# Kernel optimization log

Measured on AMD Instinct MI355X. Metric: run time of the kernel, lower is better.

Reference implementation:

```python
import jax, jax.numpy as jnp
import numpy as np

N_NODES = 100000

def gcn_conv(x, W, b, src, dst, n_nodes):
    # PyG GCNConv: out = D^{-1/2} (A + I) D^{-1/2} (x W) + b, deg includes self-loop
    h = x @ W  # [N, H]
    ones = jnp.ones(src.shape[0], dtype=x.dtype)
    deg = jax.ops.segment_sum(ones, dst, num_segments=n_nodes) + 1.0  # +1 self-loop
    dinv = jax.lax.rsqrt(deg)  # deg >= 1, no zeros
    norm = dinv[src] * dinv[dst]  # [E]
    msg = h[src] * norm[:, None]  # [E, H] gather + scale
    agg = jax.ops.segment_sum(msg, dst, num_segments=n_nodes)  # scatter-add
    self_contrib = h * (dinv * dinv)[:, None]  # self-loop term norm = dinv_i^2
    return agg + self_contrib + b


def setup_inputs() -> dict:
    key = jax.random.key(0)
    ks = jax.random.split(key, 6)
    F_IN, H, E = 128, 128, 1600000
    x = jax.random.normal(ks[0], (N_NODES, F_IN), dtype=jnp.float32)
    edge_index = jax.random.randint(ks[1], (2, E), 0, N_NODES, dtype=jnp.int32)
    s = 1.0 / np.sqrt(F_IN)
    W1 = jax.random.normal(ks[2], (F_IN, H), dtype=jnp.float32) * s
    b1 = jnp.zeros((H,), dtype=jnp.float32)
    W2 = jax.random.normal(ks[3], (H, H), dtype=jnp.float32) * (1.0 / np.sqrt(H))
    b2 = jnp.zeros((H,), dtype=jnp.float32)
    Wlin = jax.random.normal(ks[4], (H, 1), dtype=jnp.float32) * (1.0 / np.sqrt(H))
    blin = jnp.zeros((1,), dtype=jnp.float32)
    return {"x": x, "edge_index": edge_index, "W1": W1, "b1": b1,
            "W2": W2, "b2": b2, "Wlin": Wlin, "blin": blin}


def reference(x, edge_index, W1, b1, W2, b2, Wlin, blin):
    src, dst = edge_index[0], edge_index[1]
    h = gcn_conv(x, W1, b1, src, dst, N_NODES)
    h = jax.nn.relu(h)
    h = gcn_conv(h, W2, b2, src, dst, N_NODES)
    h = jax.nn.relu(h)
    out = h @ Wlin + blin  # [N, 1]
    return out.squeeze(-1)  # [N]
```

## Files before the change

kernel.cpp:

```cpp
#include <hip/hip_runtime.h>
#include <hip/hip_fp16.h>

#define NFEAT 128

typedef _Float16 v8hf __attribute__((ext_vector_type(8)));
typedef float v4f __attribute__((ext_vector_type(4)));

__global__ void k_deg_rank_w(const int* __restrict__ dst, int* __restrict__ deg,
                             int* __restrict__ rank, int E, int N,
                             const float* __restrict__ W1, const float* __restrict__ W2,
                             _Float16* __restrict__ Wt1, _Float16* __restrict__ Wt2) {
  int e = blockIdx.x * blockDim.x + threadIdx.x;
  if (e < E) rank[e] = atomicAdd(&deg[dst[e]], 1);
  else if (e < E + N) rank[e] = atomicAdd(&deg[e - E], 1);
  else if (e < E + N + 32768) {
    int idx = e - E - N;
    const float* W = (idx < 16384) ? W1 : W2;
    _Float16* Wt = (idx < 16384) ? Wt1 : Wt2;
    int i = idx & 16383;
    int k = i >> 7, n = i & 127;
    Wt[n * 128 + k] = (_Float16)W[k * 128 + n];
  }
}

__global__ __launch_bounds__(1024) void k_scan_blocks(const int* __restrict__ deg,
    int* __restrict__ base, int* __restrict__ partials, int n) {
  __shared__ int buf[1024];
  int tid = threadIdx.x;
  int i = blockIdx.x * 1024 + tid;
  int v = (i < n) ? deg[i] : 0;
  buf[tid] = v;
  __syncthreads();
  #pragma unroll
  for (int off = 1; off < 1024; off <<= 1) {
    int t = (tid >= off) ? buf[tid - off] : 0;
    __syncthreads();
    buf[tid] += t;
    __syncthreads();
  }
  if (i <= n) base[i] = buf[tid] - v;
  if (tid == 1023) partials[blockIdx.x] = buf[tid];
}

__global__ void k_scan_partials(int* __restrict__ partials, int nb) {
  __shared__ int buf[128];
  int tid = threadIdx.x;
  int v = (tid < nb) ? partials[tid] : 0;
  buf[tid] = v;
  __syncthreads();
  #pragma unroll
  for (int off = 1; off < 128; off <<= 1) {
    int t = (tid >= off) ? buf[tid - off] : 0;
    __syncthreads();
    buf[tid] += t;
    __syncthreads();
  }
  if (tid < nb) partials[tid] = buf[tid] - v;
}

__global__ void k_finalize_base(int* __restrict__ base, const int* __restrict__ partials,
    const int* __restrict__ deg, float* __restrict__ dinv, int n) {
  int i = blockIdx.x * blockDim.x + threadIdx.x;
  if (i <= n) {
    base[i] += partials[i >> 10];
    if (i < n) dinv[i] = rsqrtf((float)deg[i]);
  }
}

__global__ void k_scatter(const int* __restrict__ src, const int* __restrict__ dst,
    const int* __restrict__ rank, const int* __restrict__ base,
    int* __restrict__ ssrc, int E, int N) {
  int e = blockIdx.x * blockDim.x + threadIdx.x;
  if (e < E) ssrc[base[dst[e]] + rank[e]] = src[e];
  else if (e < E + N) { int n = e - E; ssrc[base[n] + rank[e]] = n; }
}

template <typename AT>
__global__ __launch_bounds__(256) void k_gemm_mfma(
    const AT* __restrict__ A, const _Float16* __restrict__ Wt,
    const float* __restrict__ dinv, _Float16* __restrict__ g16, int N) {
  __shared__ _Float16 As[64][136];
  __shared__ _Float16 Ws[128][136];
  const int tid = threadIdx.x;
  const int row0 = blockIdx.x * 64;

  if (blockIdx.x == 0 && tid < 16) {
    v8hf z;
    #pragma unroll
    for (int j = 0; j < 8; j++) z[j] = (_Float16)0.f;
    *(v8hf*)(g16 + (size_t)N * NFEAT + tid * 8) = z;
  }

  if constexpr (sizeof(AT) == 4) {
    #pragma unroll
    for (int i = 0; i < 8; i++) {
      int idx = tid + i * 256;
      int row = idx >> 5;
      int c4 = idx & 31;
      int gr = row0 + row; gr = (gr < N) ? gr : (N - 1);
      float4 v = *(const float4*)((const float*)A + (size_t)gr * NFEAT + c4 * 4);
      _Float16* p = &As[row][c4 * 4];
      p[0] = (_Float16)v.x; p[1] = (_Float16)v.y;
      p[2] = (_Float16)v.z; p[3] = (_Float16)v.w;
    }
  } else {
    #pragma unroll
    for (int i = 0; i < 4; i++) {
      int idx = tid + i * 256;
      int row = idx >> 4;
      int c8 = idx & 15;
      int gr = row0 + row; gr = (gr < N) ? gr : (N - 1);
      *(uint4*)&As[row][c8 * 8] =
          *(const uint4*)((const _Float16*)A + (size_t)gr * NFEAT + c8 * 8);
    }
  }
  #pragma unroll
  for (int i = 0; i < 8; i++) {
    int idx = tid + i * 256;
    int row = idx >> 4;
    int c8 = idx & 15;
    *(uint4*)&Ws[row][c8 * 8] = *(const uint4*)(Wt + (size_t)row * 128 + c8 * 8);
  }
  __syncthreads();

  const int wv = tid >> 6;
  const int lane = tid & 63;
  const int m = lane & 15;
  const int q = lane >> 4;

  v4f acc[8] = {};
  const _Float16* arow = &As[wv * 16 + m][0];
  #pragma unroll
  for (int kt = 0; kt < 4; kt++) {
    v8hf af = *(const v8hf*)(arow + kt * 32 + q * 8);
    #pragma unroll
    for (int ct = 0; ct < 8; ct++) {
      v8hf bf = *(const v8hf*)(&Ws[ct * 16 + m][kt * 32 + q * 8]);
      acc[ct] = __builtin_amdgcn_mfma_f32_16x16x32_f16(af, bf, acc[ct], 0, 0, 0);
    }
  }

  int nd[4]; float dv[4];
  #pragma unroll
  for (int r = 0; r < 4; r++) {
    nd[r] = row0 + wv * 16 + q * 4 + r;
    int c = (nd[r] < N) ? nd[r] : (N - 1);
    dv[r] = dinv[c];
  }
  #pragma unroll
  for (int ct = 0; ct < 8; ct++)
    #pragma unroll
    for (int r = 0; r < 4; r++)
      if (nd[r] < N)
        g16[(size_t)nd[r] * NFEAT + ct * 16 + m] = (_Float16)(acc[ct][r] * dv[r]);
}

__global__ __launch_bounds__(256) void k_agg(
    const _Float16* __restrict__ g, const float* __restrict__ dinv,
    const int* __restrict__ base, const int* __restrict__ ssrc,
    const float* __restrict__ bias, _Float16* __restrict__ hB, int N) {
  const int lane = threadIdx.x & 63;
  const int n = blockIdx.x * 4 + (threadIdx.x >> 6);
  if (n >= N) return;
  const int gq = lane >> 4;
  const int l = lane & 15;
  const int b0 = base[n], b1 = base[n + 1];

  int e = b0;
  int p0 = e + gq, p1 = e + 4 + gq;
  int i0 = ssrc[p0], i1 = ssrc[p1];
  i0 = (p0 < b1) ? i0 : N;
  i1 = (p1 < b1) ? i1 : N;
  v8hf r0 = *(const v8hf*)(g + (size_t)i0 * NFEAT + l * 8);
  v8hf r1 = *(const v8hf*)(g + (size_t)i1 * NFEAT + l * 8);
  int e2 = e + 8;
  int j0 = N, j1 = N;
  if (e2 < b1) {
    int q0 = e2 + gq, q1 = e2 + 4 + gq;
    j0 = ssrc[q0]; j1 = ssrc[q1];
    j0 = (q0 < b1) ? j0 : N;
    j1 = (q1 < b1) ? j1 : N;
  }

  float acc[8] = {};
  while (true) {
    bool more = (e2 < b1);
    v8hf s0, s1;
    if (more) {
      s0 = *(const v8hf*)(g + (size_t)j0 * NFEAT + l * 8);
      s1 = *(const v8hf*)(g + (size_t)j1 * NFEAT + l * 8);
    }
    int e3 = e2 + 8;
    int c0 = N, c1 = N;
    if (e3 < b1) {
      int q0 = e3 + gq, q1 = e3 + 4 + gq;
      c0 = ssrc[q0]; c1 = ssrc[q1];
      c0 = (q0 < b1) ? c0 : N;
      c1 = (q1 < b1) ? c1 : N;
    }
    #pragma unroll
    for (int j = 0; j < 8; j++) acc[j] += (float)r0[j] + (float)r1[j];
    if (!more) break;
    r0 = s0; r1 = s1;
    j0 = c0; j1 = c1;
    e2 = e3;
  }

  #pragma unroll
  for (int j = 0; j < 8; j++) {
    acc[j] += __shfl_xor(acc[j], 16, 64);
    acc[j] += __shfl_xor(acc[j], 32, 64);
  }
  if (gq == 0) {
    float dvn = dinv[n];
    const float* bp = bias + l * 8;
    float4 bb0 = *(const float4*)(bp);
    float4 bb1 = *(const float4*)(bp + 4);
    float bv[8] = {bb0.x, bb0.y, bb0.z, bb0.w, bb1.x, bb1.y, bb1.z, bb1.w};
    v8hf o;
    #pragma unroll
    for (int j = 0; j < 8; j++)
      o[j] = (_Float16)fmaxf(acc[j] * dvn + bv[j], 0.f);
    *(v8hf*)(hB + (size_t)n * NFEAT + l * 8) = o;
  }
}

__global__ __launch_bounds__(256) void k_agg_final(
    const _Float16* __restrict__ g, const float* __restrict__ dinv,
    const int* __restrict__ base, const int* __restrict__ ssrc,
    const float* __restrict__ bias, const float* __restrict__ wlin,
    const float* __restrict__ blin, float* __restrict__ out, int N) {
  const int lane = threadIdx.x & 63;
  const int n = blockIdx.x * 4 + (threadIdx.x >> 6);
  if (n >= N) return;
  const int gq = lane >> 4;
  const int l = lane & 15;
  const int b0 = base[n], b1 = base[n + 1];

  int e = b0;
  int p0 = e + gq, p1 = e + 4 + gq;
  int i0 = ssrc[p0], i1 = ssrc[p1];
  i0 = (p0 < b1) ? i0 : N;
  i1 = (p1 < b1) ? i1 : N;
  v8hf r0 = *(const v8hf*)(g + (size_t)i0 * NFEAT + l * 8);
  v8hf r1 = *(const v8hf*)(g + (size_t)i1 * NFEAT + l * 8);
  int e2 = e + 8;
  int j0 = N, j1 = N;
  if (e2 < b1) {
    int q0 = e2 + gq, q1 = e2 + 4 + gq;
    j0 = ssrc[q0]; j1 = ssrc[q1];
    j0 = (q0 < b1) ? j0 : N;
    j1 = (q1 < b1) ? j1 : N;
  }

  float acc[8] = {};
  while (true) {
    bool more = (e2 < b1);
    v8hf s0, s1;
    if (more) {
      s0 = *(const v8hf*)(g + (size_t)j0 * NFEAT + l * 8);
      s1 = *(const v8hf*)(g + (size_t)j1 * NFEAT + l * 8);
    }
    int e3 = e2 + 8;
    int c0 = N, c1 = N;
    if (e3 < b1) {
      int q0 = e3 + gq, q1 = e3 + 4 + gq;
      c0 = ssrc[q0]; c1 = ssrc[q1];
      c0 = (q0 < b1) ? c0 : N;
      c1 = (q1 < b1) ? c1 : N;
    }
    #pragma unroll
    for (int j = 0; j < 8; j++) acc[j] += (float)r0[j] + (float)r1[j];
    if (!more) break;
    r0 = s0; r1 = s1;
    j0 = c0; j1 = c1;
    e2 = e3;
  }

  #pragma unroll
  for (int j = 0; j < 8; j++) {
    acc[j] += __shfl_xor(acc[j], 16, 64);
    acc[j] += __shfl_xor(acc[j], 32, 64);
  }
  float dvn = dinv[n];
  const float* bp = bias + l * 8;
  const float* wp = wlin + l * 8;
  float4 bb0 = *(const float4*)(bp);
  float4 bb1 = *(const float4*)(bp + 4);
  float4 wl0 = *(const float4*)(wp);
  float4 wl1 = *(const float4*)(wp + 4);
  float bv[8] = {bb0.x, bb0.y, bb0.z, bb0.w, bb1.x, bb1.y, bb1.z, bb1.w};
  float wv[8] = {wl0.x, wl0.y, wl0.z, wl0.w, wl1.x, wl1.y, wl1.z, wl1.w};
  float pv = 0.f;
  #pragma unroll
  for (int j = 0; j < 8; j++)
    pv += fmaxf(acc[j] * dvn + bv[j], 0.f) * wv[j];
  pv += __shfl_xor(pv, 1, 64);
  pv += __shfl_xor(pv, 2, 64);
  pv += __shfl_xor(pv, 4, 64);
  pv += __shfl_xor(pv, 8, 64);
  if (lane == 0) out[n] = pv + blin[0];
}

extern "C" void kernel_launch(void* const* d_in, const int* in_sizes, int n_in,
                              void* d_out, int out_size, void* d_ws, size_t ws_size,
                              hipStream_t stream) {
  const float* x    = (const float*)d_in[0];
  const int*   ei   = (const int*)d_in[1];
  const float* W1   = (const float*)d_in[2];
  const float* b1   = (const float*)d_in[3];
  const float* W2   = (const float*)d_in[4];
  const float* b2   = (const float*)d_in[5];
  const float* Wlin = (const float*)d_in[6];
  const float* blin = (const float*)d_in[7];
  const int N = in_sizes[0] / NFEAT;
  const int E = in_sizes[1] / 2;
  const int* src = ei;
  const int* dst = ei + E;
  const int Etot = E + N;

  int* ws_i = (int*)d_ws;
  size_t off = 0;
  int* deg      = ws_i + off; off += N;
  int* base     = ws_i + off; off += (size_t)N + 1;
  off = (off + 3) & ~(size_t)3;
  int* partials = ws_i + off; off += 128;
  int* ssrc     = ws_i + off; off += Etot + 8;
  float* dinv   = (float*)(ws_i + off); off += N;
  off = (off + 3) & ~(size_t)3;
  _Float16* Wt1 = (_Float16*)(ws_i + off); off += 8192;
  _Float16* Wt2 = (_Float16*)(ws_i + off); off += 8192;
  _Float16* g16 = (_Float16*)(ws_i + off); off += (size_t)(N + 1) * 64;
  _Float16* hB  = (_Float16*)(ws_i + off); off += (size_t)N * 64;
  int* rank     = (int*)g16;

  hipMemsetAsync(deg, 0, (size_t)N * sizeof(int), stream);

  const int tpbE = 256;
  const int gE = (Etot + 32768 + tpbE - 1) / tpbE;
  k_deg_rank_w<<<gE, tpbE, 0, stream>>>(dst, deg, rank, E, N, W1, W2, Wt1, Wt2);

  const int nb = (N + 1 + 1023) / 1024;
  k_scan_blocks<<<nb, 1024, 0, stream>>>(deg, base, partials, N);
  k_scan_partials<<<1, 128, 0, stream>>>(partials, nb);
  k_finalize_base<<<((N + 1) + 255) / 256, 256, 0, stream>>>(base, partials, deg, dinv, N);
  k_scatter<<<(Etot + tpbE - 1) / tpbE, tpbE, 0, stream>>>(src, dst, rank, base, ssrc, E, N);

  const int gg = (N + 63) / 64;
  const int ga = (N + 3) / 4;
  k_gemm_mfma<float><<<gg, 256, 0, stream>>>(x, Wt1, dinv, g16, N);
  k_agg<<<ga, 256, 0, stream>>>(g16, dinv, base, ssrc, b1, hB, N);
  k_gemm_mfma<_Float16><<<gg, 256, 0, stream>>>(hB, Wt2, dinv, g16, N);
  k_agg_final<<<ga, 256, 0, stream>>>(g16, dinv, base, ssrc, b2,
                                      Wlin, blin, (float*)d_out, N);
}
```

Measured before the change: 383.3 us.

## Split gathered features into 16-wide column chunks for cache-local aggregation

The GEMM output is stored as eight column-chunk planes of 16 features each, and the aggregation kernels run one block per chunk, covering 16 nodes, so every gather touches a 32-byte row segment within a smaller per-chunk working set. The aim is better L2 hit rates on the random neighbor gathers, since each chunk plane is an eighth of the full feature matrix. In exchange, the index array is re-read once per chunk, the final layer needs an output memset plus atomic adds across chunks, and the per-wave loop runs to the maximum degree among the four nodes it handles.

```diff
diff --git a/kernel.cpp b/kernel.cpp
--- a/kernel.cpp
+++ b/kernel.cpp
@@ -2,6 +2,8 @@
 #include <hip/hip_fp16.h>
 
 #define NFEAT 128
+#define NCHUNK 8
+#define CFEAT 16
 
 typedef _Float16 v8hf __attribute__((ext_vector_type(8)));
 typedef float v4f __attribute__((ext_vector_type(4)));
@@ -88,7 +90,8 @@
     v8hf z;
     #pragma unroll
     for (int j = 0; j < 8; j++) z[j] = (_Float16)0.f;
-    *(v8hf*)(g16 + (size_t)N * NFEAT + tid * 8) = z;
+    int c = tid >> 1, h = tid & 1;
+    *(v8hf*)(g16 + ((size_t)c * (N + 1) + N) * CFEAT + h * 8) = z;
   }
 
   if constexpr (sizeof(AT) == 4) {
@@ -148,80 +151,79 @@
     dv[r] = dinv[c];
   }
   #pragma unroll
-  for (int ct = 0; ct < 8; ct++)
+  for (int ct = 0; ct < 8; ct++) {
+    _Float16* gout = g16 + (size_t)ct * (N + 1) * CFEAT;
     #pragma unroll
     for (int r = 0; r < 4; r++)
       if (nd[r] < N)
-        g16[(size_t)nd[r] * NFEAT + ct * 16 + m] = (_Float16)(acc[ct][r] * dv[r]);
+        gout[(size_t)nd[r] * CFEAT + m] = (_Float16)(acc[ct][r] * dv[r]);
+  }
 }
 
 __global__ __launch_bounds__(256) void k_agg(
     const _Float16* __restrict__ g, const float* __restrict__ dinv,
     const int* __restrict__ base, const int* __restrict__ ssrc,
     const float* __restrict__ bias, _Float16* __restrict__ hB, int N) {
+  const int chunk = blockIdx.x & 7;
+  const int nblk = blockIdx.x >> 3;
   const int lane = threadIdx.x & 63;
-  const int n = blockIdx.x * 4 + (threadIdx.x >> 6);
-  if (n >= N) return;
-  const int gq = lane >> 4;
-  const int l = lane & 15;
-  const int b0 = base[n], b1 = base[n + 1];
-
-  int e = b0;
-  int p0 = e + gq, p1 = e + 4 + gq;
-  int i0 = ssrc[p0], i1 = ssrc[p1];
-  i0 = (p0 < b1) ? i0 : N;
-  i1 = (p1 < b1) ? i1 : N;
-  v8hf r0 = *(const v8hf*)(g + (size_t)i0 * NFEAT + l * 8);
-  v8hf r1 = *(const v8hf*)(g + (size_t)i1 * NFEAT + l * 8);
-  int e2 = e + 8;
-  int j0 = N, j1 = N;
-  if (e2 < b1) {
-    int q0 = e2 + gq, q1 = e2 + 4 + gq;
-    j0 = ssrc[q0]; j1 = ssrc[q1];
-    j0 = (q0 < b1) ? j0 : N;
-    j1 = (q1 < b1) ? j1 : N;
-  }
+  const int wave = threadIdx.x >> 6;
+  const int half = lane & 1;
+  const int slot = (lane >> 1) & 7;
+  const int n = nblk * 16 + wave * 4 + (lane >> 4);
+
+  const _Float16* gc = g + (size_t)chunk * (N + 1) * CFEAT;
+
+  int b0 = 0, b1 = 0;
+  if (n < N) { b0 = base[n]; b1 = base[n + 1]; }
+  int nit = (b1 - b0 + 7) >> 3;
+  { int t = __shfl_xor(nit, 16, 64); nit = (t > nit) ? t : nit; }
+  { int t = __shfl_xor(nit, 32, 64); nit = (t > nit) ? t : nit; }
 
   float acc[8] = {};
-  while (true) {
-    bool more = (e2 < b1);
-    v8hf s0, s1;
-    if (more) {
-      s0 = *(const v8hf*)(g + (size_t)j0 * NFEAT + l * 8);
-      s1 = *(const v8hf*)(g + (size_t)j1 * NFEAT + l * 8);
-    }
-    int e3 = e2 + 8;
-    int c0 = N, c1 = N;
-    if (e3 < b1) {
-      int q0 = e3 + gq, q1 = e3 + 4 + gq;
-      c0 = ssrc[q0]; c1 = ssrc[q1];
-      c0 = (q0 < b1) ? c0 : N;
-      c1 = (q1 < b1) ? c1 : N;
-    }
-    #pragma unroll
-    for (int j = 0; j < 8; j++) acc[j] += (float)r0[j] + (float)r1[j];
-    if (!more) break;
-    r0 = s0; r1 = s1;
-    j0 = c0; j1 = c1;
-    e2 = e3;
-  }
-
-  #pragma unroll
-  for (int j = 0; j < 8; j++) {
-    acc[j] += __shfl_xor(acc[j], 16, 64);
-    acc[j] += __shfl_xor(acc[j], 32, 64);
-  }
-  if (gq == 0) {
+  if (nit > 0) {
+    int p = b0 + slot;
+    int i = ssrc[p];
+    i = (p < b1) ? i : N;
+    v8hf r = *(const v8hf*)(gc + (size_t)i * CFEAT + half * 8);
+    int j = N;
+    if (nit > 1) {
+      int pn = b0 + 8 + slot;
+      j = ssrc[pn];
+      j = (pn < b1) ? j : N;
+    }
+    for (int it = 1; ; ++it) {
+      bool more = (it < nit);
+      v8hf rn; int jn = N;
+      if (more) {
+        rn = *(const v8hf*)(gc + (size_t)j * CFEAT + half * 8);
+        if (it + 1 < nit) {
+          int pn = b0 + (it + 1) * 8 + slot;
+          jn = ssrc[pn];
+          jn = (pn < b1) ? jn : N;
+        }
+      }
+      #pragma unroll
+      for (int jj = 0; jj < 8; jj++) acc[jj] += (float)r[jj];
+      if (!more) break;
+      r = rn; j = jn;
+    }
+  }
+
+  #pragma unroll
+  for (int jj = 0; jj < 8; jj++) {
+    acc[jj] += __shfl_xor(acc[jj], 2, 64);
+    acc[jj] += __shfl_xor(acc[jj], 4, 64);
+    acc[jj] += __shfl_xor(acc[jj], 8, 64);
+  }
+  if (n < N && (lane & 14) == 0) {
     float dvn = dinv[n];
-    const float* bp = bias + l * 8;
-    float4 bb0 = *(const float4*)(bp);
-    float4 bb1 = *(const float4*)(bp + 4);
-    float bv[8] = {bb0.x, bb0.y, bb0.z, bb0.w, bb1.x, bb1.y, bb1.z, bb1.w};
+    const float* bp = bias + chunk * CFEAT + half * 8;
     v8hf o;
     #pragma unroll
-    for (int j = 0; j < 8; j++)
-      o[j] = (_Float16)fmaxf(acc[j] * dvn + bv[j], 0.f);
-    *(v8hf*)(hB + (size_t)n * NFEAT + l * 8) = o;
+    for (int jj = 0; jj < 8; jj++)
+      o[jj] = (_Float16)fmaxf(acc[jj] * dvn + bp[jj], 0.f);
+    *(v8hf*)(hB + (size_t)n * NFEAT + chunk * CFEAT + half * 8) = o;
   }
 }
 
@@ -230,76 +232,72 @@
     const int* __restrict__ base, const int* __restrict__ ssrc,
     const float* __restrict__ bias, const float* __restrict__ wlin,
     const float* __restrict__ blin, float* __restrict__ out, int N) {
+  const int chunk = blockIdx.x & 7;
+  const int nblk = blockIdx.x >> 3;
   const int lane = threadIdx.x & 63;
-  const int n = blockIdx.x * 4 + (threadIdx.x >> 6);
-  if (n >= N) return;
-  const int gq = lane >> 4;
-  const int l = lane & 15;
-  const int b0 = base[n], b1 = base[n + 1];
-
-  int e = b0;
-  int p0 = e + gq, p1 = e + 4 + gq;
-  int i0 = ssrc[p0], i1 = ssrc[p1];
-  i0 = (p0 < b1) ? i0 : N;
-  i1 = (p1 < b1) ? i1 : N;
-  v8hf r0 = *(const v8hf*)(g + (size_t)i0 * NFEAT + l * 8);
-  v8hf r1 = *(const v8hf*)(g + (size_t)i1 * NFEAT + l * 8);
-  int e2 = e + 8;
-  int j0 = N, j1 = N;
-  if (e2 < b1) {
-    int q0 = e2 + gq, q1 = e2 + 4 + gq;
-    j0 = ssrc[q0]; j1 = ssrc[q1];
-    j0 = (q0 < b1) ? j0 : N;
-    j1 = (q1 < b1) ? j1 : N;
-  }
+  const int wave = threadIdx.x >> 6;
+  const int half = lane & 1;
+  const int slot = (lane >> 1) & 7;
+  const int n = nblk * 16 + wave * 4 + (lane >> 4);
+
+  const _Float16* gc = g + (size_t)chunk * (N + 1) * CFEAT;
+
+  int b0 = 0, b1 = 0;
+  if (n < N) { b0 = base[n]; b1 = base[n + 1]; }
+  int nit = (b1 - b0 + 7) >> 3;
+  { int t = __shfl_xor(nit, 16, 64); nit = (t > nit) ? t : nit; }
+  { int t = __shfl_xor(nit, 32, 64); nit = (t > nit) ? t : nit; }
 
   float acc[8] = {};
-  while (true) {
-    bool more = (e2 < b1);
-    v8hf s0, s1;
-    if (more) {
-      s0 = *(const v8hf*)(g + (size_t)j0 * NFEAT + l * 8);
-      s1 = *(const v8hf*)(g + (size_t)j1 * NFEAT + l * 8);
-    }
-    int e3 = e2 + 8;
-    int c0 = N, c1 = N;
-    if (e3 < b1) {
-      int q0 = e3 + gq, q1 = e3 + 4 + gq;
-      c0 = ssrc[q0]; c1 = ssrc[q1];
-      c0 = (q0 < b1) ? c0 : N;
-      c1 = (q1 < b1) ? c1 : N;
-    }
-    #pragma unroll
-    for (int j = 0; j < 8; j++) acc[j] += (float)r0[j] + (float)r1[j];
-    if (!more) break;
-    r0 = s0; r1 = s1;
-    j0 = c0; j1 = c1;
-    e2 = e3;
-  }
-
-  #pragma unroll
-  for (int j = 0; j < 8; j++) {
-    acc[j] += __shfl_xor(acc[j], 16, 64);
-    acc[j] += __shfl_xor(acc[j], 32, 64);
-  }
-  float dvn = dinv[n];
-  const float* bp = bias + l * 8;
-  const float* wp = wlin + l * 8;
-  float4 bb0 = *(const float4*)(bp);
-  float4 bb1 = *(const float4*)(bp + 4);
-  float4 wl0 = *(const float4*)(wp);
-  float4 wl1 = *(const float4*)(wp + 4);
-  float bv[8] = {bb0.x, bb0.y, bb0.z, bb0.w, bb1.x, bb1.y, bb1.z, bb1.w};
-  float wv[8] = {wl0.x, wl0.y, wl0.z, wl0.w, wl1.x, wl1.y, wl1.z, wl1.w};
+  if (nit > 0) {
+    int p = b0 + slot;
+    int i = ssrc[p];
+    i = (p < b1) ? i : N;
+    v8hf r = *(const v8hf*)(gc + (size_t)i * CFEAT + half * 8);
+    int j = N;
+    if (nit > 1) {
+      int pn = b0 + 8 + slot;
+      j = ssrc[pn];
+      j = (pn < b1) ? j : N;
+    }
+    for (int it = 1; ; ++it) {
+      bool more = (it < nit);
+      v8hf rn; int jn = N;
+      if (more) {
+        rn = *(const v8hf*)(gc + (size_t)j * CFEAT + half * 8);
+        if (it + 1 < nit) {
+          int pn = b0 + (it + 1) * 8 + slot;
+          jn = ssrc[pn];
+          jn = (pn < b1) ? jn : N;
+        }
+      }
+      #pragma unroll
+      for (int jj = 0; jj < 8; jj++) acc[jj] += (float)r[jj];
+      if (!more) break;
+      r = rn; j = jn;
+    }
+  }
+
+  #pragma unroll
+  for (int jj = 0; jj < 8; jj++) {
+    acc[jj] += __shfl_xor(acc[jj], 2, 64);
+    acc[jj] += __shfl_xor(acc[jj], 4, 64);
+    acc[jj] += __shfl_xor(acc[jj], 8, 64);
+  }
   float pv = 0.f;
-  #pragma unroll
-  for (int j = 0; j < 8; j++)
-    pv += fmaxf(acc[j] * dvn + bv[j], 0.f) * wv[j];
+  if (n < N) {
+    float dvn = dinv[n];
+    const float* bp = bias + chunk * CFEAT + half * 8;
+    const float* wp = wlin + chunk * CFEAT + half * 8;
+    #pragma unroll
+    for (int jj = 0; jj < 8; jj++)
+      pv += fmaxf(acc[jj] * dvn + bp[jj], 0.f) * wp[jj];
+  }
   pv += __shfl_xor(pv, 1, 64);
-  pv += __shfl_xor(pv, 2, 64);
-  pv += __shfl_xor(pv, 4, 64);
-  pv += __shfl_xor(pv, 8, 64);
-  if (lane == 0) out[n] = pv + blin[0];
+  if (n < N && (lane & 15) == 0) {
+    if (chunk == 0) pv += blin[0];
+    atomicAdd(out + n, pv);
+  }
 }
 
 extern "C" void kernel_launch(void* const* d_in, const int* in_sizes, int n_in,
@@ -325,7 +323,7 @@
   int* base     = ws_i + off; off += (size_t)N + 1;
   off = (off + 3) & ~(size_t)3;
   int* partials = ws_i + off; off += 128;
-  int* ssrc     = ws_i + off; off += Etot + 8;
+  int* ssrc     = ws_i + off; off += Etot + 64;
   float* dinv   = (float*)(ws_i + off); off += N;
   off = (off + 3) & ~(size_t)3;
   _Float16* Wt1 = (_Float16*)(ws_i + off); off += 8192;
@@ -335,6 +333,7 @@
   int* rank     = (int*)g16;
 
   hipMemsetAsync(deg, 0, (size_t)N * sizeof(int), stream);
+  hipMemsetAsync(d_out, 0, (size_t)N * sizeof(float), stream);
 
   const int tpbE = 256;
   const int gE = (Etot + 32768 + tpbE - 1) / tpbE;
@@ -347,7 +346,7 @@
   k_scatter<<<(Etot + tpbE - 1) / tpbE, tpbE, 0, stream>>>(src, dst, rank, base, ssrc, E, N);
 
   const int gg = (N + 63) / 64;
-  const int ga = (N + 3) / 4;
+  const int ga = NCHUNK * ((N + 15) >> 4);
   k_gemm_mfma<float><<<gg, 256, 0, stream>>>(x, Wt1, dinv, g16, N);
   k_agg<<<ga, 256, 0, stream>>>(g16, dinv, base, ssrc, b1, hB, N);
   k_gemm_mfma<_Float16><<<gg, 256, 0, stream>>>(hB, Wt2, dinv, g16, N);
```

Result: slower. 438.7 us (+14.5%).

## Fuse all GCN stages into one cooperative persistent kernel with grid syncs

Applied to the files above, without the earlier changes.

Replaces the chain of nine kernel launches (degree/rank, three scan stages, scatter, two GEMMs, two aggregations) with a single cooperative kernel of 512 persistent blocks that loops over work and separates stages with grid.sync. The scan is redone with 512-element chunks using wave shuffles. The goal is to remove launch gaps and tail effects between the many small stages. The trade-off is a fixed grid size that limits occupancy per phase, plus grid barrier costs, and a fallback to the old launches if the cooperative launch fails.

```diff
diff --git a/kernel.cpp b/kernel.cpp
--- a/kernel.cpp
+++ b/kernel.cpp
@@ -1,10 +1,351 @@
 #include <hip/hip_runtime.h>
 #include <hip/hip_fp16.h>
+#include <hip/hip_cooperative_groups.h>
+
+namespace cg = cooperative_groups;
 
 #define NFEAT 128
+#define NBLK 512
 
 typedef _Float16 v8hf __attribute__((ext_vector_type(8)));
 typedef float v4f __attribute__((ext_vector_type(4)));
+
+__device__ __forceinline__ int wave_incl_scan(int v, int lane) {
+  #pragma unroll
+  for (int off = 1; off < 64; off <<= 1) {
+    int t = __shfl_up(v, off, 64);
+    if (lane >= off) v += t;
+  }
+  return v;
+}
+
+template <typename AT>
+__device__ __forceinline__ void gemm_tile(
+    const AT* A, const _Float16* Wt, const float* dinv,
+    _Float16* g16, int N, int tile,
+    _Float16 (*As)[136], _Float16 (*Ws)[136]) {
+  const int tid = threadIdx.x;
+  const int row0 = tile * 64;
+
+  if constexpr (sizeof(AT) == 4) {
+    #pragma unroll
+    for (int i = 0; i < 8; i++) {
+      int idx = tid + i * 256;
+      int row = idx >> 5;
+      int c4 = idx & 31;
+      int gr = row0 + row; gr = (gr < N) ? gr : (N - 1);
+      float4 v = *(const float4*)((const float*)A + (size_t)gr * NFEAT + c4 * 4);
+      _Float16* p = &As[row][c4 * 4];
+      p[0] = (_Float16)v.x; p[1] = (_Float16)v.y;
+      p[2] = (_Float16)v.z; p[3] = (_Float16)v.w;
+    }
+  } else {
+    #pragma unroll
+    for (int i = 0; i < 4; i++) {
+      int idx = tid + i * 256;
+      int row = idx >> 4;
+      int c8 = idx & 15;
+      int gr = row0 + row; gr = (gr < N) ? gr : (N - 1);
+      *(uint4*)&As[row][c8 * 8] =
+          *(const uint4*)((const _Float16*)A + (size_t)gr * NFEAT + c8 * 8);
+    }
+  }
+  #pragma unroll
+  for (int i = 0; i < 8; i++) {
+    int idx = tid + i * 256;
+    int row = idx >> 4;
+    int c8 = idx & 15;
+    *(uint4*)&Ws[row][c8 * 8] = *(const uint4*)(Wt + (size_t)row * 128 + c8 * 8);
+  }
+  __syncthreads();
+
+  const int wv = tid >> 6;
+  const int lane = tid & 63;
+  const int m = lane & 15;
+  const int q = lane >> 4;
+
+  v4f acc[8] = {};
+  const _Float16* arow = &As[wv * 16 + m][0];
+  #pragma unroll
+  for (int kt = 0; kt < 4; kt++) {
+    v8hf af = *(const v8hf*)(arow + kt * 32 + q * 8);
+    #pragma unroll
+    for (int ct = 0; ct < 8; ct++) {
+      v8hf bf = *(const v8hf*)(&Ws[ct * 16 + m][kt * 32 + q * 8]);
+      acc[ct] = __builtin_amdgcn_mfma_f32_16x16x32_f16(af, bf, acc[ct], 0, 0, 0);
+    }
+  }
+
+  int nd[4]; float dv[4];
+  #pragma unroll
+  for (int r = 0; r < 4; r++) {
+    nd[r] = row0 + wv * 16 + q * 4 + r;
+    int c = (nd[r] < N) ? nd[r] : (N - 1);
+    dv[r] = dinv[c];
+  }
+  #pragma unroll
+  for (int ct = 0; ct < 8; ct++)
+    #pragma unroll
+    for (int r = 0; r < 4; r++)
+      if (nd[r] < N)
+        g16[(size_t)nd[r] * NFEAT + ct * 16 + m] = (_Float16)(acc[ct][r] * dv[r]);
+}
+
+__device__ __forceinline__ void agg_node(
+    const _Float16* g, const float* dinv, const int* base, const int* ssrc,
+    const float* bias, _Float16* hB, int N, int n) {
+  const int lane = threadIdx.x & 63;
+  if (n >= N) return;
+  const int gq = lane >> 4;
+  const int l = lane & 15;
+  const int b0 = base[n], b1 = base[n + 1];
+
+  int e = b0;
+  int p0 = e + gq, p1 = e + 4 + gq;
+  int i0 = ssrc[p0], i1 = ssrc[p1];
+  i0 = (p0 < b1) ? i0 : N;
+  i1 = (p1 < b1) ? i1 : N;
+  v8hf r0 = *(const v8hf*)(g + (size_t)i0 * NFEAT + l * 8);
+  v8hf r1 = *(const v8hf*)(g + (size_t)i1 * NFEAT + l * 8);
+  int e2 = e + 8;
+  int j0 = N, j1 = N;
+  if (e2 < b1) {
+    int q0 = e2 + gq, q1 = e2 + 4 + gq;
+    j0 = ssrc[q0]; j1 = ssrc[q1];
+    j0 = (q0 < b1) ? j0 : N;
+    j1 = (q1 < b1) ? j1 : N;
+  }
+
+  float acc[8] = {};
+  while (true) {
+    bool more = (e2 < b1);
+    v8hf s0, s1;
+    if (more) {
+      s0 = *(const v8hf*)(g + (size_t)j0 * NFEAT + l * 8);
+      s1 = *(const v8hf*)(g + (size_t)j1 * NFEAT + l * 8);
+    }
+    int e3 = e2 + 8;
+    int c0 = N, c1 = N;
+    if (e3 < b1) {
+      int q0 = e3 + gq, q1 = e3 + 4 + gq;
+      c0 = ssrc[q0]; c1 = ssrc[q1];
+      c0 = (q0 < b1) ? c0 : N;
+      c1 = (q1 < b1) ? c1 : N;
+    }
+    #pragma unroll
+    for (int j = 0; j < 8; j++) acc[j] += (float)r0[j] + (float)r1[j];
+    if (!more) break;
+    r0 = s0; r1 = s1;
+    j0 = c0; j1 = c1;
+    e2 = e3;
+  }
+
+  #pragma unroll
+  for (int j = 0; j < 8; j++) {
+    acc[j] += __shfl_xor(acc[j], 16, 64);
+    acc[j] += __shfl_xor(acc[j], 32, 64);
+  }
+  if (gq == 0) {
+    float dvn = dinv[n];
+    const float* bp = bias + l * 8;
+    float4 bb0 = *(const float4*)(bp);
+    float4 bb1 = *(const float4*)(bp + 4);
+    float bv[8] = {bb0.x, bb0.y, bb0.z, bb0.w, bb1.x, bb1.y, bb1.z, bb1.w};
+    v8hf o;
+    #pragma unroll
+    for (int j = 0; j < 8; j++)
+      o[j] = (_Float16)fmaxf(acc[j] * dvn + bv[j], 0.f);
+    *(v8hf*)(hB + (size_t)n * NFEAT + l * 8) = o;
+  }
+}
+
+__device__ __forceinline__ void agg_final_node(
+    const _Float16* g, const float* dinv, const int* base, const int* ssrc,
+    const float* bias, const float* wlin, const float* blin,
+    float* out, int N, int n) {
+  const int lane = threadIdx.x & 63;
+  if (n >= N) return;
+  const int gq = lane >> 4;
+  const int l = lane & 15;
+  const int b0 = base[n], b1 = base[n + 1];
+
+  int e = b0;
+  int p0 = e + gq, p1 = e + 4 + gq;
+  int i0 = ssrc[p0], i1 = ssrc[p1];
+  i0 = (p0 < b1) ? i0 : N;
+  i1 = (p1 < b1) ? i1 : N;
+  v8hf r0 = *(const v8hf*)(g + (size_t)i0 * NFEAT + l * 8);
+  v8hf r1 = *(const v8hf*)(g + (size_t)i1 * NFEAT + l * 8);
+  int e2 = e + 8;
+  int j0 = N, j1 = N;
+  if (e2 < b1) {
+    int q0 = e2 + gq, q1 = e2 + 4 + gq;
+    j0 = ssrc[q0]; j1 = ssrc[q1];
+    j0 = (q0 < b1) ? j0 : N;
+    j1 = (q1 < b1) ? j1 : N;
+  }
+
+  float acc[8] = {};
+  while (true) {
+    bool more = (e2 < b1);
+    v8hf s0, s1;
+    if (more) {
+      s0 = *(const v8hf*)(g + (size_t)j0 * NFEAT + l * 8);
+      s1 = *(const v8hf*)(g + (size_t)j1 * NFEAT + l * 8);
+    }
+    int e3 = e2 + 8;
+    int c0 = N, c1 = N;
+    if (e3 < b1) {
+      int q0 = e3 + gq, q1 = e3 + 4 + gq;
+      c0 = ssrc[q0]; c1 = ssrc[q1];
+      c0 = (q0 < b1) ? c0 : N;
+      c1 = (q1 < b1) ? c1 : N;
+    }
+    #pragma unroll
+    for (int j = 0; j < 8; j++) acc[j] += (float)r0[j] + (float)r1[j];
+    if (!more) break;
+    r0 = s0; r1 = s1;
+    j0 = c0; j1 = c1;
+    e2 = e3;
+  }
+
+  #pragma unroll
+  for (int j = 0; j < 8; j++) {
+    acc[j] += __shfl_xor(acc[j], 16, 64);
+    acc[j] += __shfl_xor(acc[j], 32, 64);
+  }
+  float dvn = dinv[n];
+  const float* bp = bias + l * 8;
+  const float* wp = wlin + l * 8;
+  float4 bb0 = *(const float4*)(bp);
+  float4 bb1 = *(const float4*)(bp + 4);
+  float4 wl0 = *(const float4*)(wp);
+  float4 wl1 = *(const float4*)(wp + 4);
+  float bv[8] = {bb0.x, bb0.y, bb0.z, bb0.w, bb1.x, bb1.y, bb1.z, bb1.w};
+  float wv[8] = {wl0.x, wl0.y, wl0.z, wl0.w, wl1.x, wl1.y, wl1.z, wl1.w};
+  float pv = 0.f;
+  #pragma unroll
+  for (int j = 0; j < 8; j++)
+    pv += fmaxf(acc[j] * dvn + bv[j], 0.f) * wv[j];
+  pv += __shfl_xor(pv, 1, 64);
+  pv += __shfl_xor(pv, 2, 64);
+  pv += __shfl_xor(pv, 4, 64);
+  pv += __shfl_xor(pv, 8, 64);
+  if (lane == 0) out[n] = pv + blin[0];
+}
+
+__global__ __launch_bounds__(256, 2) void k_mega(
+    const float* __restrict__ x, const int* __restrict__ ei,
+    const float* __restrict__ W1, const float* __restrict__ b1,
+    const float* __restrict__ W2, const float* __restrict__ b2,
+    const float* __restrict__ Wlin, const float* __restrict__ blin,
+    int* deg, int* base, int* partials, int* ssrc, float* dinv,
+    _Float16* Wt1, _Float16* Wt2, _Float16* g16, _Float16* hB,
+    float* out, int E, int N) {
+  __shared__ _Float16 As[64][136];
+  __shared__ _Float16 Ws[128][136];
+  __shared__ int scan_lds[4];
+  cg::grid_group grid = cg::this_grid();
+
+  const int tid = threadIdx.x;
+  const int lane = tid & 63;
+  const int wv = tid >> 6;
+  const int gid = blockIdx.x * 256 + tid;
+  const int gstride = gridDim.x * 256;
+  const int Etot = E + N;
+  const int* src = ei;
+  const int* dst = ei + E;
+  int* rank = (int*)g16;
+
+  for (int e = gid; e < Etot + 32768; e += gstride) {
+    if (e < E) rank[e] = atomicAdd(&deg[dst[e]], 1);
+    else if (e < Etot) rank[e] = atomicAdd(&deg[e - E], 1);
+    else {
+      int idx = e - Etot;
+      const float* W = (idx < 16384) ? W1 : W2;
+      _Float16* Wt = (idx < 16384) ? Wt1 : Wt2;
+      int i = idx & 16383;
+      int k = i >> 7, nn = i & 127;
+      Wt[nn * 128 + k] = (_Float16)W[k * 128 + nn];
+    }
+  }
+  grid.sync();
+
+  const int N1 = N + 1;
+  const int nch = (N1 + 511) >> 9;
+  for (int ch = blockIdx.x; ch < nch; ch += gridDim.x) {
+    int i0 = (ch << 9) + (tid << 1);
+    int a = (i0 < N) ? deg[i0] : 0;
+    int b = (i0 + 1 < N) ? deg[i0 + 1] : 0;
+    int inc = wave_incl_scan(a + b, lane);
+    if (lane == 63) scan_lds[wv] = inc;
+    __syncthreads();
+    int woff = 0, tot = 0;
+    #pragma unroll
+    for (int w = 0; w < 4; w++) {
+      int t = scan_lds[w];
+      tot += t;
+      if (w < wv) woff += t;
+    }
+    __syncthreads();
+    int ex = woff + inc - (a + b);
+    if (i0 < N1) base[i0] = ex;
+    if (i0 + 1 < N1) base[i0 + 1] = ex + a;
+    if (tid == 0) partials[ch] = tot;
+  }
+  grid.sync();
+
+  if (blockIdx.x == 0) {
+    int v = (tid < nch) ? partials[tid] : 0;
+    int inc = wave_incl_scan(v, lane);
+    if (lane == 63) scan_lds[wv] = inc;
+    __syncthreads();
+    int woff = 0;
+    #pragma unroll
+    for (int w = 0; w < 4; w++) if (w < wv) woff += scan_lds[w];
+    if (tid < nch) partials[tid] = woff + inc - v;
+  }
+  grid.sync();
+
+  for (int i = gid; i < N1; i += gstride) {
+    base[i] += partials[i >> 9];
+    if (i < N) dinv[i] = rsqrtf((float)deg[i]);
+  }
+  if (blockIdx.x == 0 && tid < 16) {
+    v8hf z;
+    #pragma unroll
+    for (int j = 0; j < 8; j++) z[j] = (_Float16)0.f;
+    *(v8hf*)(g16 + (size_t)N * NFEAT + tid * 8) = z;
+  }
+  grid.sync();
+
+  for (int e = gid; e < Etot; e += gstride) {
+    if (e < E) ssrc[base[dst[e]] + rank[e]] = src[e];
+    else { int nn = e - E; ssrc[base[nn] + rank[e]] = nn; }
+  }
+  grid.sync();
+
+  const int ntiles = (N + 63) >> 6;
+  for (int t = blockIdx.x; t < ntiles; t += gridDim.x) {
+    __syncthreads();
+    gemm_tile<float>(x, Wt1, dinv, g16, N, t, As, Ws);
+  }
+  grid.sync();
+
+  const int ngrp = (N + 3) >> 2;
+  for (int g4 = blockIdx.x; g4 < ngrp; g4 += gridDim.x)
+    agg_node(g16, dinv, base, ssrc, b1, hB, N, g4 * 4 + wv);
+  grid.sync();
+
+  for (int t = blockIdx.x; t < ntiles; t += gridDim.x) {
+    __syncthreads();
+    gemm_tile<_Float16>(hB, Wt2, dinv, g16, N, t, As, Ws);
+  }
+  grid.sync();
+
+  for (int g4 = blockIdx.x; g4 < ngrp; g4 += gridDim.x)
+    agg_final_node(g16, dinv, base, ssrc, b2, Wlin, blin, out, N, g4 * 4 + wv);
+}
 
 __global__ void k_deg_rank_w(const int* __restrict__ dst, int* __restrict__ deg,
                              int* __restrict__ rank, int E, int N,
@@ -81,148 +422,20 @@
     const float* __restrict__ dinv, _Float16* __restrict__ g16, int N) {
   __shared__ _Float16 As[64][136];
   __shared__ _Float16 Ws[128][136];
-  const int tid = threadIdx.x;
-  const int row0 = blockIdx.x * 64;
-
-  if (blockIdx.x == 0 && tid < 16) {
+  if (blockIdx.x == 0 && threadIdx.x < 16) {
     v8hf z;
     #pragma unroll
     for (int j = 0; j < 8; j++) z[j] = (_Float16)0.f;
-    *(v8hf*)(g16 + (size_t)N * NFEAT + tid * 8) = z;
-  }
-
-  if constexpr (sizeof(AT) == 4) {
-    #pragma unroll
-    for (int i = 0; i < 8; i++) {
-      int idx = tid + i * 256;
-      int row = idx >> 5;
-      int c4 = idx & 31;
-      int gr = row0 + row; gr = (gr < N) ? gr : (N - 1);
-      float4 v = *(const float4*)((const float*)A + (size_t)gr * NFEAT + c4 * 4);
-      _Float16* p = &As[row][c4 * 4];
-      p[0] = (_Float16)v.x; p[1] = (_Float16)v.y;
-      p[2] = (_Float16)v.z; p[3] = (_Float16)v.w;
-    }
-  } else {
-    #pragma unroll
-    for (int i = 0; i < 4; i++) {
-      int idx = tid + i * 256;
-      int row = idx >> 4;
-      int c8 = idx & 15;
-      int gr = row0 + row; gr = (gr < N) ? gr : (N - 1);
-      *(uint4*)&As[row][c8 * 8] =
-          *(const uint4*)((const _Float16*)A + (size_t)gr * NFEAT + c8 * 8);
-    }
-  }
-  #pragma unroll
-  for (int i = 0; i < 8; i++) {
-    int idx = tid + i * 256;
-    int row = idx >> 4;
-    int c8 = idx & 15;
-    *(uint4*)&Ws[row][c8 * 8] = *(const uint4*)(Wt + (size_t)row * 128 + c8 * 8);
-  }
-  __syncthreads();
-
-  const int wv = tid >> 6;
-  const int lane = tid & 63;
-  const int m = lane & 15;
-  const int q = lane >> 4;
-
-  v4f acc[8] = {};
-  const _Float16* arow = &As[wv * 16 + m][0];
-  #pragma unroll
-  for (int kt = 0; kt < 4; kt++) {
-    v8hf af = *(const v8hf*)(arow + kt * 32 + q * 8);
-    #pragma unroll
-    for (int ct = 0; ct < 8; ct++) {
-      v8hf bf = *(const v8hf*)(&Ws[ct * 16 + m][kt * 32 + q * 8]);
-      acc[ct] = __builtin_amdgcn_mfma_f32_16x16x32_f16(af, bf, acc[ct], 0, 0, 0);
-    }
-  }
-
-  int nd[4]; float dv[4];
-  #pragma unroll
-  for (int r = 0; r < 4; r++) {
-    nd[r] = row0 + wv * 16 + q * 4 + r;
-    int c = (nd[r] < N) ? nd[r] : (N - 1);
-    dv[r] = dinv[c];
-  }
-  #pragma unroll
-  for (int ct = 0; ct < 8; ct++)
-    #pragma unroll
-    for (int r = 0; r < 4; r++)
-      if (nd[r] < N)
-        g16[(size_t)nd[r] * NFEAT + ct * 16 + m] = (_Float16)(acc[ct][r] * dv[r]);
+    *(v8hf*)(g16 + (size_t)N * NFEAT + threadIdx.x * 8) = z;
+  }
+  gemm_tile<AT>(A, Wt, dinv, g16, N, blockIdx.x, As, Ws);
 }
 
 __global__ __launch_bounds__(256) void k_agg(
     const _Float16* __restrict__ g, const float* __restrict__ dinv,
     const int* __restrict__ base, const int* __restrict__ ssrc,
     const float* __restrict__ bias, _Float16* __restrict__ hB, int N) {
-  const int lane = threadIdx.x & 63;
-  const int n = blockIdx.x * 4 + (threadIdx.x >> 6);
-  if (n >= N) return;
-  const int gq = lane >> 4;
-  const int l = lane & 15;
-  const int b0 = base[n], b1 = base[n + 1];
-
-  int e = b0;
-  int p0 = e + gq, p1 = e + 4 + gq;
-  int i0 = ssrc[p0], i1 = ssrc[p1];
-  i0 = (p0 < b1) ? i0 : N;
-  i1 = (p1 < b1) ? i1 : N;
-  v8hf r0 = *(const v8hf*)(g + (size_t)i0 * NFEAT + l * 8);
-  v8hf r1 = *(const v8hf*)(g + (size_t)i1 * NFEAT + l * 8);
-  int e2 = e + 8;
-  int j0 = N, j1 = N;
-  if (e2 < b1) {
-    int q0 = e2 + gq, q1 = e2 + 4 + gq;
-    j0 = ssrc[q0]; j1 = ssrc[q1];
-    j0 = (q0 < b1) ? j0 : N;
-    j1 = (q1 < b1) ? j1 : N;
-  }
-
-  float acc[8] = {};
-  while (true) {
-    bool more = (e2 < b1);
-    v8hf s0, s1;
-    if (more) {
-      s0 = *(const v8hf*)(g + (size_t)j0 * NFEAT + l * 8);
-      s1 = *(const v8hf*)(g + (size_t)j1 * NFEAT + l * 8);
-    }
-    int e3 = e2 + 8;
-    int c0 = N, c1 = N;
-    if (e3 < b1) {
-      int q0 = e3 + gq, q1 = e3 + 4 + gq;
-      c0 = ssrc[q0]; c1 = ssrc[q1];
-      c0 = (q0 < b1) ? c0 : N;
-      c1 = (q1 < b1) ? c1 : N;
-    }
-    #pragma unroll
-    for (int j = 0; j < 8; j++) acc[j] += (float)r0[j] + (float)r1[j];
-    if (!more) break;
-    r0 = s0; r1 = s1;
-    j0 = c0; j1 = c1;
-    e2 = e3;
-  }
-
-  #pragma unroll
-  for (int j = 0; j < 8; j++) {
-    acc[j] += __shfl_xor(acc[j], 16, 64);
-    acc[j] += __shfl_xor(acc[j], 32, 64);
-  }
-  if (gq == 0) {
-    float dvn = dinv[n];
-    const float* bp = bias + l * 8;
-    float4 bb0 = *(const float4*)(bp);
-    float4 bb1 = *(const float4*)(bp + 4);
-    float bv[8] = {bb0.x, bb0.y, bb0.z, bb0.w, bb1.x, bb1.y, bb1.z, bb1.w};
-    v8hf o;
-    #pragma unroll
-    for (int j = 0; j < 8; j++)
-      o[j] = (_Float16)fmaxf(acc[j] * dvn + bv[j], 0.f);
-    *(v8hf*)(hB + (size_t)n * NFEAT + l * 8) = o;
-  }
+  agg_node(g, dinv, base, ssrc, bias, hB, N, blockIdx.x * 4 + (threadIdx.x >> 6));
 }
 
 __global__ __launch_bounds__(256) void k_agg_final(
@@ -230,76 +443,8 @@
     const int* __restrict__ base, const int* __restrict__ ssrc,
     const float* __restrict__ bias, const float* __restrict__ wlin,
     const float* __restrict__ blin, float* __restrict__ out, int N) {
-  const int lane = threadIdx.x & 63;
-  const int n = blockIdx.x * 4 + (threadIdx.x >> 6);
-  if (n >= N) return;
-  const int gq = lane >> 4;
-  const int l = lane & 15;
-  const int b0 = base[n], b1 = base[n + 1];
-
-  int e = b0;
-  int p0 = e + gq, p1 = e + 4 + gq;
-  int i0 = ssrc[p0], i1 = ssrc[p1];
-  i0 = (p0 < b1) ? i0 : N;
-  i1 = (p1 < b1) ? i1 : N;
-  v8hf r0 = *(const v8hf*)(g + (size_t)i0 * NFEAT + l * 8);
-  v8hf r1 = *(const v8hf*)(g + (size_t)i1 * NFEAT + l * 8);
-  int e2 = e + 8;
-  int j0 = N, j1 = N;
-  if (e2 < b1) {
-    int q0 = e2 + gq, q1 = e2 + 4 + gq;
-    j0 = ssrc[q0]; j1 = ssrc[q1];
-    j0 = (q0 < b1) ? j0 : N;
-    j1 = (q1 < b1) ? j1 : N;
-  }
-
-  float acc[8] = {};
-  while (true) {
-    bool more = (e2 < b1);
-    v8hf s0, s1;
-    if (more) {
-      s0 = *(const v8hf*)(g + (size_t)j0 * NFEAT + l * 8);
-      s1 = *(const v8hf*)(g + (size_t)j1 * NFEAT + l * 8);
-    }
-    int e3 = e2 + 8;
-    int c0 = N, c1 = N;
-    if (e3 < b1) {
-      int q0 = e3 + gq, q1 = e3 + 4 + gq;
-      c0 = ssrc[q0]; c1 = ssrc[q1];
-      c0 = (q0 < b1) ? c0 : N;
-      c1 = (q1 < b1) ? c1 : N;
-    }
-    #pragma unroll
-    for (int j = 0; j < 8; j++) acc[j] += (float)r0[j] + (float)r1[j];
-    if (!more) break;
-    r0 = s0; r1 = s1;
-    j0 = c0; j1 = c1;
-    e2 = e3;
-  }
-
-  #pragma unroll
-  for (int j = 0; j < 8; j++) {
-    acc[j] += __shfl_xor(acc[j], 16, 64);
-    acc[j] += __shfl_xor(acc[j], 32, 64);
-  }
-  float dvn = dinv[n];
-  const float* bp = bias + l * 8;
-  const float* wp = wlin + l * 8;
-  float4 bb0 = *(const float4*)(bp);
-  float4 bb1 = *(const float4*)(bp + 4);
-  float4 wl0 = *(const float4*)(wp);
-  float4 wl1 = *(const float4*)(wp + 4);
-  float bv[8] = {bb0.x, bb0.y, bb0.z, bb0.w, bb1.x, bb1.y, bb1.z, bb1.w};
-  float wv[8] = {wl0.x, wl0.y, wl0.z, wl0.w, wl1.x, wl1.y, wl1.z, wl1.w};
-  float pv = 0.f;
-  #pragma unroll
-  for (int j = 0; j < 8; j++)
-    pv += fmaxf(acc[j] * dvn + bv[j], 0.f) * wv[j];
-  pv += __shfl_xor(pv, 1, 64);
-  pv += __shfl_xor(pv, 2, 64);
-  pv += __shfl_xor(pv, 4, 64);
-  pv += __shfl_xor(pv, 8, 64);
-  if (lane == 0) out[n] = pv + blin[0];
+  agg_final_node(g, dinv, base, ssrc, bias, wlin, blin, out, N,
+                 blockIdx.x * 4 + (threadIdx.x >> 6));
 }
 
 extern "C" void kernel_launch(void* const* d_in, const int* in_sizes, int n_in,
@@ -315,16 +460,15 @@
   const float* blin = (const float*)d_in[7];
   const int N = in_sizes[0] / NFEAT;
   const int E = in_sizes[1] / 2;
-  const int* src = ei;
-  const int* dst = ei + E;
   const int Etot = E + N;
+  float* outp = (float*)d_out;
 
   int* ws_i = (int*)d_ws;
   size_t off = 0;
   int* deg      = ws_i + off; off += N;
   int* base     = ws_i + off; off += (size_t)N + 1;
   off = (off + 3) & ~(size_t)3;
-  int* partials = ws_i + off; off += 128;
+  int* partials = ws_i + off; off += 256;
   int* ssrc     = ws_i + off; off += Etot + 8;
   float* dinv   = (float*)(ws_i + off); off += N;
   off = (off + 3) & ~(size_t)3;
@@ -336,21 +480,34 @@
 
   hipMemsetAsync(deg, 0, (size_t)N * sizeof(int), stream);
 
-  const int tpbE = 256;
-  const int gE = (Etot + 32768 + tpbE - 1) / tpbE;
-  k_deg_rank_w<<<gE, tpbE, 0, stream>>>(dst, deg, rank, E, N, W1, W2, Wt1, Wt2);
-
-  const int nb = (N + 1 + 1023) / 1024;
-  k_scan_blocks<<<nb, 1024, 0, stream>>>(deg, base, partials, N);
-  k_scan_partials<<<1, 128, 0, stream>>>(partials, nb);
-  k_finalize_base<<<((N + 1) + 255) / 256, 256, 0, stream>>>(base, partials, deg, dinv, N);
-  k_scatter<<<(Etot + tpbE - 1) / tpbE, tpbE, 0, stream>>>(src, dst, rank, base, ssrc, E, N);
-
-  const int gg = (N + 63) / 64;
-  const int ga = (N + 3) / 4;
-  k_gemm_mfma<float><<<gg, 256, 0, stream>>>(x, Wt1, dinv, g16, N);
-  k_agg<<<ga, 256, 0, stream>>>(g16, dinv, base, ssrc, b1, hB, N);
-  k_gemm_mfma<_Float16><<<gg, 256, 0, stream>>>(hB, Wt2, dinv, g16, N);
-  k_agg_final<<<ga, 256, 0, stream>>>(g16, dinv, base, ssrc, b2,
-                                      Wlin, blin, (float*)d_out, N);
-}
+  int Ea = E, Na = N;
+  void* args[] = {
+    (void*)&x, (void*)&ei, (void*)&W1, (void*)&b1, (void*)&W2, (void*)&b2,
+    (void*)&Wlin, (void*)&blin, (void*)&deg, (void*)&base, (void*)&partials,
+    (void*)&ssrc, (void*)&dinv, (void*)&Wt1, (void*)&Wt2, (void*)&g16,
+    (void*)&hB, (void*)&outp, (void*)&Ea, (void*)&Na
+  };
+  hipError_t err = hipLaunchCooperativeKernel(k_mega, dim3(NBLK), dim3(256),
+                                              args, 0, stream);
+  if (err != hipSuccess) {
+    const int* src = ei;
+    const int* dst = ei + E;
+    const int tpbE = 256;
+    const int gE = (Etot + 32768 + tpbE - 1) / tpbE;
+    k_deg_rank_w<<<gE, tpbE, 0, stream>>>(dst, deg, rank, E, N, W1, W2, Wt1, Wt2);
+
+    const int nb = (N + 1 + 1023) / 1024;
+    k_scan_blocks<<<nb, 1024, 0, stream>>>(deg, base, partials, N);
+    k_scan_partials<<<1, 128, 0, stream>>>(partials, nb);
+    k_finalize_base<<<((N + 1) + 255) / 256, 256, 0, stream>>>(base, partials, deg, dinv, N);
+    k_scatter<<<(Etot + tpbE - 1) / tpbE, tpbE, 0, stream>>>(src, dst, rank, base, ssrc, E, N);
+
+    const int gg = (N + 63) / 64;
+    const int ga = (N + 3) / 4;
+    k_gemm_mfma<float><<<gg, 256, 0, stream>>>(x, Wt1, dinv, g16, N);
+    k_agg<<<ga, 256, 0, stream>>>(g16, dinv, base, ssrc, b1, hB, N);
+    k_gemm_mfma<_Float16><<<gg, 256, 0, stream>>>(hB, Wt2, dinv, g16, N);
+    k_agg_final<<<ga, 256, 0, stream>>>(g16, dinv, base, ssrc, b2,
+                                        Wlin, blin, outp, N);
+  }
+}
```

New measurement: 964.3 us. +151.6%, slower.

## Use wave-shuffle scans and stage GEMM output through LDS for coalesced stores

Applied to the files above, without the earlier changes.

The block scan moves from an LDS Hillis-Steele loop with many barriers to 64-wide wave shuffle scans over 256-thread blocks, with each thread handling two elements. The partials scan is rewritten the same way. The GEMM epilogue now writes scaled fp16 results into shared memory and then stores 16-byte vectors per row, replacing scattered 2-byte global stores, and the fp32-to-fp16 A-tile conversion uses one vector LDS store. These changes target scan synchronisation overhead and uncoalesced GEMM writes, at the cost of two extra barriers in the GEMM.

```diff
diff --git a/kernel.cpp b/kernel.cpp
--- a/kernel.cpp
+++ b/kernel.cpp
@@ -4,6 +4,7 @@
 #define NFEAT 128
 
 typedef _Float16 v8hf __attribute__((ext_vector_type(8)));
+typedef _Float16 v4hf __attribute__((ext_vector_type(4)));
 typedef float v4f __attribute__((ext_vector_type(4)));
 
 __global__ void k_deg_rank_w(const int* __restrict__ dst, int* __restrict__ deg,
@@ -23,46 +24,62 @@
   }
 }
 
-__global__ __launch_bounds__(1024) void k_scan_blocks(const int* __restrict__ deg,
+__device__ __forceinline__ int wave_incl_scan(int v, int lane) {
+  #pragma unroll
+  for (int off = 1; off < 64; off <<= 1) {
+    int t = __shfl_up(v, off, 64);
+    if (lane >= off) v += t;
+  }
+  return v;
+}
+
+__global__ __launch_bounds__(256) void k_scan_blocks(const int* __restrict__ deg,
     int* __restrict__ base, int* __restrict__ partials, int n) {
-  __shared__ int buf[1024];
-  int tid = threadIdx.x;
-  int i = blockIdx.x * 1024 + tid;
-  int v = (i < n) ? deg[i] : 0;
-  buf[tid] = v;
-  __syncthreads();
-  #pragma unroll
-  for (int off = 1; off < 1024; off <<= 1) {
-    int t = (tid >= off) ? buf[tid - off] : 0;
-    __syncthreads();
-    buf[tid] += t;
-    __syncthreads();
-  }
-  if (i <= n) base[i] = buf[tid] - v;
-  if (tid == 1023) partials[blockIdx.x] = buf[tid];
-}
-
-__global__ void k_scan_partials(int* __restrict__ partials, int nb) {
-  __shared__ int buf[128];
-  int tid = threadIdx.x;
+  __shared__ int lds[4];
+  const int tid = threadIdx.x;
+  const int lane = tid & 63;
+  const int wv = tid >> 6;
+  int i0 = (blockIdx.x << 9) + (tid << 1);
+  int a = (i0 < n) ? deg[i0] : 0;
+  int b = (i0 + 1 < n) ? deg[i0 + 1] : 0;
+  int inc = wave_incl_scan(a + b, lane);
+  if (lane == 63) lds[wv] = inc;
+  __syncthreads();
+  int woff = 0, tot = 0;
+  #pragma unroll
+  for (int w = 0; w < 4; w++) {
+    int t = lds[w];
+    tot += t;
+    if (w < wv) woff += t;
+  }
+  int ex = woff + inc - (a + b);
+  const int N1 = n + 1;
+  if (i0 < N1) base[i0] = ex;
+  if (i0 + 1 < N1) base[i0 + 1] = ex + a;
+  if (tid == 255) partials[blockIdx.x] = tot;
+}
+
+__global__ __launch_bounds__(256) void k_scan_partials(int* __restrict__ partials,
+                                                       int nb) {
+  __shared__ int lds[4];
+  const int tid = threadIdx.x;
+  const int lane = tid & 63;
+  const int wv = tid >> 6;
   int v = (tid < nb) ? partials[tid] : 0;
-  buf[tid] = v;
-  __syncthreads();
-  #pragma unroll
-  for (int off = 1; off < 128; off <<= 1) {
-    int t = (tid >= off) ? buf[tid - off] : 0;
-    __syncthreads();
-    buf[tid] += t;
-    __syncthreads();
-  }
-  if (tid < nb) partials[tid] = buf[tid] - v;
+  int inc = wave_incl_scan(v, lane);
+  if (lane == 63) lds[wv] = inc;
+  __syncthreads();
+  int woff = 0;
+  #pragma unroll
+  for (int w = 0; w < 4; w++) if (w < wv) woff += lds[w];
+  if (tid < nb) partials[tid] = woff + inc - v;
 }
 
 __global__ void k_finalize_base(int* __restrict__ base, const int* __restrict__ partials,
     const int* __restrict__ deg, float* __restrict__ dinv, int n) {
   int i = blockIdx.x * blockDim.x + threadIdx.x;
   if (i <= n) {
-    base[i] += partials[i >> 10];
+    base[i] += partials[i >> 9];
     if (i < n) dinv[i] = rsqrtf((float)deg[i]);
   }
 }
@@ -99,9 +116,10 @@
       int c4 = idx & 31;
       int gr = row0 + row; gr = (gr < N) ? gr : (N - 1);
       float4 v = *(const float4*)((const float*)A + (size_t)gr * NFEAT + c4 * 4);
-      _Float16* p = &As[row][c4 * 4];
-      p[0] = (_Float16)v.x; p[1] = (_Float16)v.y;
-      p[2] = (_Float16)v.z; p[3] = (_Float16)v.w;
+      v4hf h;
+      h[0] = (_Float16)v.x; h[1] = (_Float16)v.y;
+      h[2] = (_Float16)v.z; h[3] = (_Float16)v.w;
+      *(v4hf*)&As[row][c4 * 4] = h;
     }
   } else {
     #pragma unroll
@@ -140,19 +158,31 @@
     }
   }
 
-  int nd[4]; float dv[4];
+  float dv[4];
   #pragma unroll
   for (int r = 0; r < 4; r++) {
-    nd[r] = row0 + wv * 16 + q * 4 + r;
-    int c = (nd[r] < N) ? nd[r] : (N - 1);
+    int nd = row0 + wv * 16 + q * 4 + r;
+    int c = (nd < N) ? nd : (N - 1);
     dv[r] = dinv[c];
   }
+
+  __syncthreads();
   #pragma unroll
   for (int ct = 0; ct < 8; ct++)
     #pragma unroll
     for (int r = 0; r < 4; r++)
-      if (nd[r] < N)
-        g16[(size_t)nd[r] * NFEAT + ct * 16 + m] = (_Float16)(acc[ct][r] * dv[r]);
+      As[wv * 16 + q * 4 + r][ct * 16 + m] = (_Float16)(acc[ct][r] * dv[r]);
+  __syncthreads();
+
+  #pragma unroll
+  for (int i = 0; i < 4; i++) {
+    int idx = tid + i * 256;
+    int row = idx >> 4;
+    int c8 = idx & 15;
+    int gr = row0 + row;
+    if (gr < N)
+      *(v8hf*)(g16 + (size_t)gr * NFEAT + c8 * 8) = *(const v8hf*)&As[row][c8 * 8];
+  }
 }
 
 __global__ __launch_bounds__(256) void k_agg(
@@ -324,7 +354,7 @@
   int* deg      = ws_i + off; off += N;
   int* base     = ws_i + off; off += (size_t)N + 1;
   off = (off + 3) & ~(size_t)3;
-  int* partials = ws_i + off; off += 128;
+  int* partials = ws_i + off; off += 256;
   int* ssrc     = ws_i + off; off += Etot + 8;
   float* dinv   = (float*)(ws_i + off); off += N;
   off = (off + 3) & ~(size_t)3;
@@ -340,9 +370,9 @@
   const int gE = (Etot + 32768 + tpbE - 1) / tpbE;
   k_deg_rank_w<<<gE, tpbE, 0, stream>>>(dst, deg, rank, E, N, W1, W2, Wt1, Wt2);
 
-  const int nb = (N + 1 + 1023) / 1024;
-  k_scan_blocks<<<nb, 1024, 0, stream>>>(deg, base, partials, N);
-  k_scan_partials<<<1, 128, 0, stream>>>(partials, nb);
+  const int nb = (N + 1 + 511) / 512;
+  k_scan_blocks<<<nb, 256, 0, stream>>>(deg, base, partials, N);
+  k_scan_partials<<<1, 256, 0, stream>>>(partials, nb);
   k_finalize_base<<<((N + 1) + 255) / 256, 256, 0, stream>>>(base, partials, deg, dinv, N);
   k_scatter<<<(Etot + tpbE - 1) / tpbE, tpbE, 0, stream>>>(src, dst, rank, base, ssrc, E, N);
 
```

Measured after the change: 373.6 us. -2.5%, faster.
